# Optimization experiments

Measured on AMD Instinct MI355X. Metric: run time of the kernel, lower is better.

The kernel has to match this reference:

```python
import jax, jax.numpy as jnp
import numpy as np

E, K = 8, 2            # num_experts, top_k
D, H = 1024, 4096      # d_model, expert_hidden_dim
B, S = 4, 2048         # batch, seq
AUX_W = 0.01


def setup_inputs() -> dict:
    key = jax.random.key(0)
    k0, k1, k2, k3 = jax.random.split(key, 4)
    return {
        "x": jax.random.normal(k0, (B, S, D), jnp.float32),
        "router_w": jax.random.normal(k1, (D, E), jnp.float32) * 0.02,  # normal(0.02) init per MoERouter
        "router_b": jnp.zeros((E,), jnp.float32),
        "w_up": jax.random.normal(k2, (E, D, H), jnp.float32) * (1.0 / np.sqrt(D)),
        "b_up": jnp.zeros((E, H), jnp.float32),
        "w_down": jax.random.normal(k3, (E, H, D), jnp.float32) * (1.0 / np.sqrt(H)),
        "b_down": jnp.zeros((E, D), jnp.float32),
    }


def reference(x, router_w, router_b, w_up, b_up, w_down, b_down):
    # Router
    logits = x @ router_w + router_b                       # (B,S,E)
    router_probs = jax.nn.softmax(logits, axis=-1)         # (B,S,E)
    topk_logits, topk_idx = jax.lax.top_k(logits, K)       # (B,S,K)
    topk_p = jax.nn.softmax(topk_logits, axis=-1)          # (B,S,K)

    # Dense all-expert MLP (matches original: every expert computed on every token)
    h = jax.nn.gelu(jnp.einsum('bsd,edh->bseh', x, w_up) + b_up)   # (B,S,E,H)
    all_out = jnp.einsum('bseh,ehd->bsed', h, w_down) + b_down     # (B,S,E,D)

    # Top-k gather + weighted combine
    sel = jnp.take_along_axis(all_out, topk_idx[..., None], axis=2)  # (B,S,K,D)
    output = jnp.sum(topk_p[..., None] * sel, axis=2)                # (B,S,D)

    # Load-balancing aux loss (Switch/Mixtral formulation)
    counts = jnp.zeros((E,), jnp.float32).at[topk_idx.reshape(-1)].add(1.0)
    fraction = counts / (B * S * K)
    prob_mean = router_probs.mean(axis=(0, 1))
    aux_loss = E * jnp.sum(fraction * prob_mean) * AUX_W
    return output, aux_loss, router_probs
```

## Files before the change

### kernel.cpp

```cpp
#include <hip/hip_runtime.h>
#include <hip/hip_bf16.h>
#include <stdint.h>

constexpr int NT = 8192;
constexpr int NE = 8;
constexpr int ND = 1024;
constexpr int NH = 4096;

typedef __attribute__((ext_vector_type(8))) short short8;
typedef __attribute__((ext_vector_type(4))) float f32x4;

constexpr size_t O_XBF  = 0;
constexpr size_t O_WUPT = O_XBF  + (size_t)NT * ND * 2;
constexpr size_t O_WDNT = O_WUPT + (size_t)NE * NH * ND * 2;
constexpr size_t O_HBUF = O_WDNT + (size_t)NE * ND * NH * 2;
constexpr size_t O_STOK = O_HBUF + (size_t)NT * 2 * NH * 2;
constexpr size_t O_SP   = O_STOK + (size_t)NT * 2 * 4;
constexpr size_t O_TKE  = O_SP   + (size_t)NT * 2 * 4;
constexpr size_t O_TKP  = O_TKE  + (size_t)NT * 2 * 4;
constexpr size_t O_CTRL = O_TKP  + (size_t)NT * 2 * 4;
constexpr size_t O_TLUP = O_CTRL + 272;
constexpr size_t O_TLDN = O_TLUP + 144 * 4;

__device__ __forceinline__ void gl_lds16(const void* g, void* l) {
  using GP = char __attribute__((address_space(1))) *;
  using LP = char __attribute__((address_space(3))) *;
  __builtin_amdgcn_global_load_lds((GP)(uintptr_t)g, (LP)(uint32_t)(uintptr_t)l, 16, 0, 0);
}

__device__ __forceinline__ float fast_gelu(float x) {
  float u  = 0.7978845608028654f * (x + 0.044715f * x * x * x);
  float ex = __expf(2.0f * u);
  float th = 1.0f - 2.0f / (ex + 1.0f);
  return 0.5f * x * (1.0f + th);
}

__global__ __launch_bounds__(256) void moe_router(
    const float* __restrict__ x, const float* __restrict__ rw, const float* __restrict__ rb,
    __hip_bfloat16* __restrict__ xbf,
    float* __restrict__ probs_out, int* __restrict__ topk_e, float* __restrict__ topk_p,
    int* __restrict__ cnt_ek, float* __restrict__ probsum)
{
  __shared__ float ps[NE];
  __shared__ int cs[16];
  const int tid = threadIdx.x;
  if (tid < NE) ps[tid] = 0.f;
  if (tid < 16) cs[tid] = 0;
  __syncthreads();
  const int lane = tid & 63, wv = tid >> 6;
  for (int it = 0; it < 8; ++it) {
    const int t = blockIdx.x * 4 + wv + it * 1024;
    const float* xr = x + (size_t)t * ND;
    float acc[NE] = {};
#pragma unroll 4
    for (int j = 0; j < 16; ++j) {
      const int d = j * 64 + lane;
      const float xv = xr[d];
      xbf[(size_t)t * ND + d] = __float2bfloat16(xv);
      const float* w = rw + (size_t)d * NE;
#pragma unroll
      for (int ee = 0; ee < NE; ++ee) acc[ee] += xv * w[ee];
    }
#pragma unroll
    for (int ee = 0; ee < NE; ++ee)
#pragma unroll
      for (int off = 32; off >= 1; off >>= 1)
        acc[ee] += __shfl_down(acc[ee], off, 64);
    if (lane == 0) {
      float lg[NE];
#pragma unroll
      for (int ee = 0; ee < NE; ++ee) lg[ee] = acc[ee] + rb[ee];
      float mx = lg[0];
#pragma unroll
      for (int ee = 1; ee < NE; ++ee) mx = fmaxf(mx, lg[ee]);
      float s = 0.f, pe[NE];
#pragma unroll
      for (int ee = 0; ee < NE; ++ee) { pe[ee] = __expf(lg[ee] - mx); s += pe[ee]; }
      const float inv = 1.f / s;
#pragma unroll
      for (int ee = 0; ee < NE; ++ee) {
        const float pr = pe[ee] * inv;
        probs_out[(size_t)t * NE + ee] = pr;
        atomicAdd(&ps[ee], pr);
      }
      int i1 = 0; float l1 = lg[0];
#pragma unroll
      for (int ee = 1; ee < NE; ++ee) if (lg[ee] > l1) { l1 = lg[ee]; i1 = ee; }
      int i2 = 0; float l2 = -3.0e38f;
#pragma unroll
      for (int ee = 0; ee < NE; ++ee) if (ee != i1 && lg[ee] > l2) { l2 = lg[ee]; i2 = ee; }
      const float e2 = __expf(l2 - l1);
      const float dn = 1.f + e2;
      topk_e[t * 2]     = i1;  topk_e[t * 2 + 1] = i2;
      topk_p[t * 2]     = 1.f / dn;
      topk_p[t * 2 + 1] = e2 / dn;
      atomicAdd(&cs[i1 * 2], 1);
      atomicAdd(&cs[i2 * 2 + 1], 1);
    }
  }
  __syncthreads();
  if (tid < NE) atomicAdd(&probsum[tid], ps[tid]);
  if (tid < 16) atomicAdd(&cnt_ek[tid], cs[tid]);
}

__global__ void moe_finalize(const int* __restrict__ cnt_ek, int* __restrict__ off_ek,
                             const float* __restrict__ probsum, float* __restrict__ aux_out,
                             int* __restrict__ ntiles, int* __restrict__ tl_up,
                             int* __restrict__ tl_dn)
{
  if (threadIdx.x == 0 && blockIdx.x == 0) {
    int run = 0;
    for (int i = 0; i < 16; ++i) { off_ek[i] = run; run += cnt_ek[i]; }
    float aux = 0.f;
    for (int ee = 0; ee < NE; ++ee) {
      float frac = (float)(cnt_ek[2 * ee] + cnt_ek[2 * ee + 1]) / (float)(NT * 2);
      aux += frac * (probsum[ee] / (float)NT);
    }
    aux_out[0] = (float)NE * aux * 0.01f;
    int ntu = 0;
    for (int e = 0; e < NE; ++e) {
      const int c = cnt_ek[2 * e] + cnt_ek[2 * e + 1];
      for (int mb = 0; mb < (c + 127) / 128; ++mb) tl_up[ntu++] = (e << 16) | mb;
    }
    ntiles[0] = ntu;
    for (int kp = 0; kp < 2; ++kp) {
      int nt = 0;
      for (int e = 0; e < NE; ++e) {
        const int c = cnt_ek[2 * e + kp];
        for (int mb = 0; mb < (c + 127) / 128; ++mb) tl_dn[kp * 80 + nt++] = (e << 16) | mb;
      }
      ntiles[1 + kp] = nt;
    }
  }
}

__global__ __launch_bounds__(256) void moe_scatter(
    const int* __restrict__ topk_e, const float* __restrict__ topk_p,
    const int* __restrict__ off_ek, int* __restrict__ fill_ek,
    int* __restrict__ slot_token, float* __restrict__ slot_p)
{
  const int t = blockIdx.x * 256 + threadIdx.x;
  if (t >= NT) return;
#pragma unroll
  for (int k = 0; k < 2; ++k) {
    const int ee = topk_e[t * 2 + k];
    const int id = ee * 2 + k;
    const int r = atomicAdd(&fill_ek[id], 1);
    const int slot = off_ek[id] + r;
    slot_token[slot] = t;
    slot_p[slot] = topk_p[t * 2 + k];
  }
}

__global__ __launch_bounds__(256) void moe_transpose_cast(
    const float* __restrict__ in, __hip_bfloat16* __restrict__ outp, int Adim, int Bdim)
{
  __shared__ unsigned short tile[64 * 66];
  const int e = blockIdx.z;
  const int b0 = blockIdx.x * 64, a0 = blockIdx.y * 64;
  const float* ip = in + (size_t)e * Adim * Bdim + (size_t)a0 * Bdim + b0;
  const int c4 = (threadIdx.x & 15) * 4;
  const int r0 = threadIdx.x >> 4;
#pragma unroll
  for (int i = 0; i < 4; ++i) {
    const int r = r0 + i * 16;
    const float4 v = *(const float4*)(ip + (size_t)r * Bdim + c4);
    ushort4 u;
    u.x = __hip_bfloat16_raw(__float2bfloat16(v.x)).x;
    u.y = __hip_bfloat16_raw(__float2bfloat16(v.y)).x;
    u.z = __hip_bfloat16_raw(__float2bfloat16(v.z)).x;
    u.w = __hip_bfloat16_raw(__float2bfloat16(v.w)).x;
    *(ushort4*)&tile[r * 66 + c4] = u;
  }
  __syncthreads();
  unsigned short* op = (unsigned short*)outp + (size_t)e * Bdim * Adim + (size_t)b0 * Adim + a0;
  const int cc  = threadIdx.x >> 2;
  const int rr0 = (threadIdx.x & 3) * 16;
  unsigned short u[16];
#pragma unroll
  for (int i = 0; i < 16; ++i) u[i] = tile[(rr0 + i) * 66 + cc];
  *(short8*)(op + (size_t)cc * Adim + rr0)     = *(short8*)&u[0];
  *(short8*)(op + (size_t)cc * Adim + rr0 + 8) = *(short8*)&u[8];
}

__global__ __launch_bounds__(512, 5) void moe_gemm_up(
    const __hip_bfloat16* __restrict__ xbf,
    const __hip_bfloat16* __restrict__ wupT,
    const float* __restrict__ b_up,
    const int* __restrict__ slot_token,
    const int* __restrict__ cnt_ek, const int* __restrict__ off_ek,
    const int* __restrict__ ntiles, const int* __restrict__ tl_up,
    __hip_bfloat16* __restrict__ hbuf)
{
  if ((int)blockIdx.y >= ntiles[0]) return;
  const int tl = tl_up[blockIdx.y];
  const int e = tl >> 16, mb = tl & 0xffff;
  const int cnt = cnt_ek[2 * e] + cnt_ek[2 * e + 1];
  const int base = off_ek[2 * e];
  const int m0 = mb * 128;
  const int n0 = blockIdx.x * 128;
  const int valid = (cnt - m0 < 128) ? (cnt - m0) : 128;

  __shared__ __align__(16) __hip_bfloat16 As[128 * 32];
  __shared__ __align__(16) __hip_bfloat16 Bs[128 * 32];

  const int tid = threadIdx.x;
  const int lane = tid & 63, wv = tid >> 6;

  const int ra = tid >> 2;
  const int kc = ((tid & 3) ^ ((ra >> 1) & 3)) * 8;
  const int sa = base + ((m0 + ra < cnt) ? (m0 + ra) : (cnt - 1));
  const __hip_bfloat16* ga = xbf + (size_t)slot_token[sa] * ND + kc;
  const __hip_bfloat16* gb = wupT + ((size_t)e * NH + n0 + ra) * ND + kc;
  char* lA = (char*)As + tid * 16;
  char* lB = (char*)Bs + tid * 16;

  const int wm = (wv >> 2) * 64, wn = (wv & 3) * 32;
  const int l15 = lane & 15, q = lane >> 4;
  const int ssw = (q ^ ((l15 >> 1) & 3)) * 16;
  const char* rA = (const char*)As + (wm + l15) * 64 + ssw;
  const char* rB = (const char*)Bs + (wn + l15) * 64 + ssw;

  f32x4 acc[4][2] = {};

  for (int kk = 0; kk < ND; kk += 32) {
    __syncthreads();
    gl_lds16(ga + kk, lA);
    gl_lds16(gb + kk, lB);
    __syncthreads();
    short8 af[4], bfr[2];
#pragma unroll
    for (int i = 0; i < 4; ++i) af[i]  = *(const short8*)(rA + i * 1024);
#pragma unroll
    for (int i = 0; i < 2; ++i) bfr[i] = *(const short8*)(rB + i * 1024);
#pragma unroll
    for (int mt = 0; mt < 4; ++mt)
#pragma unroll
      for (int nt = 0; nt < 2; ++nt)
        acc[mt][nt] = __builtin_amdgcn_mfma_f32_16x16x32_bf16(af[mt], bfr[nt], acc[mt][nt], 0, 0, 0);
  }

#pragma unroll
  for (int mt = 0; mt < 4; ++mt) {
#pragma unroll
    for (int rr = 0; rr < 4; ++rr) {
      const int row = wm + mt * 16 + q * 4 + rr;
      if (row < valid) {
        const size_t rbase = (size_t)(base + m0 + row) * NH;
#pragma unroll
        for (int nt = 0; nt < 2; ++nt) {
          const int col = n0 + wn + nt * 16 + l15;
          const float v = acc[mt][nt][rr] + b_up[e * NH + col];
          hbuf[rbase + col] = __float2bfloat16(fast_gelu(v));
        }
      }
    }
  }
}

__global__ __launch_bounds__(512, 5) void moe_gemm_down(
    const __hip_bfloat16* __restrict__ hbuf,
    const __hip_bfloat16* __restrict__ wdnT,
    const float* __restrict__ b_down,
    const int* __restrict__ slot_token, const float* __restrict__ slot_p,
    const int* __restrict__ cnt_ek, const int* __restrict__ off_ek,
    const int* __restrict__ ntiles, const int* __restrict__ tl_dn,
    float* __restrict__ out, int kpos)
{
  if ((int)blockIdx.y >= ntiles[1 + kpos]) return;
  const int tl = tl_dn[kpos * 80 + blockIdx.y];
  const int e = tl >> 16, mb = tl & 0xffff;
  const int id = 2 * e + kpos;
  const int cnt = cnt_ek[id];
  const int base = off_ek[id];
  const int m0 = mb * 128;
  const int n0 = blockIdx.x * 128;
  const int valid = (cnt - m0 < 128) ? (cnt - m0) : 128;

  __shared__ __align__(16) __hip_bfloat16 As[128 * 32];
  __shared__ __align__(16) __hip_bfloat16 Bs[128 * 32];

  const int tid = threadIdx.x;
  const int lane = tid & 63, wv = tid >> 6;

  const int ra = tid >> 2;
  const int kc = ((tid & 3) ^ ((ra >> 1) & 3)) * 8;
  const int sa = base + ((m0 + ra < cnt) ? (m0 + ra) : (cnt - 1));
  const __hip_bfloat16* ga = hbuf + (size_t)sa * NH + kc;
  const __hip_bfloat16* gb = wdnT + ((size_t)e * ND + n0 + ra) * NH + kc;
  char* lA = (char*)As + tid * 16;
  char* lB = (char*)Bs + tid * 16;

  const int wm = (wv >> 2) * 64, wn = (wv & 3) * 32;
  const int l15 = lane & 15, q = lane >> 4;
  const int ssw = (q ^ ((l15 >> 1) & 3)) * 16;
  const char* rA = (const char*)As + (wm + l15) * 64 + ssw;
  const char* rB = (const char*)Bs + (wn + l15) * 64 + ssw;

  f32x4 acc[4][2] = {};

  for (int kk = 0; kk < NH; kk += 32) {
    __syncthreads();
    gl_lds16(ga + kk, lA);
    gl_lds16(gb + kk, lB);
    __syncthreads();
    short8 af[4], bfr[2];
#pragma unroll
    for (int i = 0; i < 4; ++i) af[i]  = *(const short8*)(rA + i * 1024);
#pragma unroll
    for (int i = 0; i < 2; ++i) bfr[i] = *(const short8*)(rB + i * 1024);
#pragma unroll
    for (int mt = 0; mt < 4; ++mt)
#pragma unroll
      for (int nt = 0; nt < 2; ++nt)
        acc[mt][nt] = __builtin_amdgcn_mfma_f32_16x16x32_bf16(af[mt], bfr[nt], acc[mt][nt], 0, 0, 0);
  }

#pragma unroll
  for (int mt = 0; mt < 4; ++mt) {
#pragma unroll
    for (int rr = 0; rr < 4; ++rr) {
      const int row = wm + mt * 16 + q * 4 + rr;
      if (row < valid) {
        const int slot = base + m0 + row;
        const int tok = slot_token[slot];
        const float p = slot_p[slot];
        const size_t obase = (size_t)tok * ND;
#pragma unroll
        for (int nt = 0; nt < 2; ++nt) {
          const int col = n0 + wn + nt * 16 + l15;
          const float v = (acc[mt][nt][rr] + b_down[e * ND + col]) * p;
          if (kpos == 0) out[obase + col] = v;
          else           out[obase + col] += v;
        }
      }
    }
  }
}

extern "C" void kernel_launch(void* const* d_in, const int* in_sizes, int n_in,
                              void* d_out, int out_size, void* d_ws, size_t ws_size,
                              hipStream_t stream) {
  (void)in_sizes; (void)n_in; (void)out_size; (void)ws_size;
  const float* x   = (const float*)d_in[0];
  const float* rw  = (const float*)d_in[1];
  const float* rb  = (const float*)d_in[2];
  const float* wup = (const float*)d_in[3];
  const float* bup = (const float*)d_in[4];
  const float* wdn = (const float*)d_in[5];
  const float* bdn = (const float*)d_in[6];
  float* out = (float*)d_out;

  char* ws = (char*)d_ws;
  __hip_bfloat16* xbf  = (__hip_bfloat16*)(ws + O_XBF);
  __hip_bfloat16* wupT = (__hip_bfloat16*)(ws + O_WUPT);
  __hip_bfloat16* wdnT = (__hip_bfloat16*)(ws + O_WDNT);
  __hip_bfloat16* hbuf = (__hip_bfloat16*)(ws + O_HBUF);
  int*   slot_token = (int*)(ws + O_STOK);
  float* slot_p     = (float*)(ws + O_SP);
  int*   topk_e     = (int*)(ws + O_TKE);
  float* topk_p     = (float*)(ws + O_TKP);
  int*   cnt_ek  = (int*)(ws + O_CTRL);
  int*   fill_ek = (int*)(ws + O_CTRL + 64);
  float* probsum = (float*)(ws + O_CTRL + 128);
  int*   off_ek  = (int*)(ws + O_CTRL + 192);
  int*   ntiles  = (int*)(ws + O_CTRL + 256);
  int*   tl_up   = (int*)(ws + O_TLUP);
  int*   tl_dn   = (int*)(ws + O_TLDN);

  hipMemsetAsync(ws + O_CTRL, 0, 272, stream);

  moe_transpose_cast<<<dim3(NH / 64, ND / 64, NE), 256, 0, stream>>>(wup, wupT, ND, NH);
  moe_transpose_cast<<<dim3(ND / 64, NH / 64, NE), 256, 0, stream>>>(wdn, wdnT, NH, ND);

  moe_router<<<256, 256, 0, stream>>>(x, rw, rb, xbf, out + (size_t)NT * ND + 1,
                                      topk_e, topk_p, cnt_ek, probsum);
  moe_finalize<<<1, 64, 0, stream>>>(cnt_ek, off_ek, probsum, out + (size_t)NT * ND,
                                     ntiles, tl_up, tl_dn);
  moe_scatter<<<NT / 256, 256, 0, stream>>>(topk_e, topk_p, off_ek, fill_ek, slot_token, slot_p);

  moe_gemm_up<<<dim3(NH / 128, 144, 1), 512, 0, stream>>>(xbf, wupT, bup, slot_token,
                                                          cnt_ek, off_ek, ntiles, tl_up, hbuf);
  moe_gemm_down<<<dim3(ND / 128, 80, 1), 512, 0, stream>>>(hbuf, wdnT, bdn, slot_token, slot_p,
                                                           cnt_ek, off_ek, ntiles, tl_dn, out, 0);
  moe_gemm_down<<<dim3(ND / 128, 80, 1), 512, 0, stream>>>(hbuf, wdnT, bdn, slot_token, slot_p,
                                                           cnt_ek, off_ek, ntiles, tl_dn, out, 1);
}
```

Before: 933.2 us.

## Use 192x192x64 tiles with 32x32 MFMA and merge down-proj launches via atomics

New measurement: 1.108 ms. 1.19x slower.

```diff
diff --git a/kernel.cpp b/kernel.cpp
--- a/kernel.cpp
+++ b/kernel.cpp
@@ -7,8 +7,13 @@
 constexpr int ND = 1024;
 constexpr int NH = 4096;
 
-typedef __attribute__((ext_vector_type(8))) short short8;
-typedef __attribute__((ext_vector_type(4))) float f32x4;
+constexpr int TM = 192;
+constexpr int TN = 192;
+constexpr int BK = 64;
+
+typedef __attribute__((ext_vector_type(8)))  short short8;
+typedef __attribute__((ext_vector_type(16))) float f32x16;
+typedef __attribute__((ext_vector_type(4)))  float f32x4;
 
 constexpr size_t O_XBF  = 0;
 constexpr size_t O_WUPT = O_XBF  + (size_t)NT * ND * 2;
@@ -20,7 +25,7 @@
 constexpr size_t O_TKP  = O_TKE  + (size_t)NT * 2 * 4;
 constexpr size_t O_CTRL = O_TKP  + (size_t)NT * 2 * 4;
 constexpr size_t O_TLUP = O_CTRL + 272;
-constexpr size_t O_TLDN = O_TLUP + 144 * 4;
+constexpr size_t O_TLDN = O_TLUP + 96 * 4;
 
 __device__ __forceinline__ void gl_lds16(const void* g, void* l) {
   using GP = char __attribute__((address_space(1))) *;
@@ -120,17 +125,16 @@
     int ntu = 0;
     for (int e = 0; e < NE; ++e) {
       const int c = cnt_ek[2 * e] + cnt_ek[2 * e + 1];
-      for (int mb = 0; mb < (c + 127) / 128; ++mb) tl_up[ntu++] = (e << 16) | mb;
+      for (int mb = 0; mb < (c + TM - 1) / TM; ++mb) tl_up[ntu++] = (e << 20) | mb;
     }
     ntiles[0] = ntu;
-    for (int kp = 0; kp < 2; ++kp) {
-      int nt = 0;
+    int nt = 0;
+    for (int kp = 0; kp < 2; ++kp)
       for (int e = 0; e < NE; ++e) {
         const int c = cnt_ek[2 * e + kp];
-        for (int mb = 0; mb < (c + 127) / 128; ++mb) tl_dn[kp * 80 + nt++] = (e << 16) | mb;
+        for (int mb = 0; mb < (c + TM - 1) / TM; ++mb) tl_dn[nt++] = (e << 20) | (kp << 16) | mb;
       }
-      ntiles[1 + kp] = nt;
-    }
+    ntiles[1] = nt;
   }
 }
 
@@ -183,7 +187,7 @@
   *(short8*)(op + (size_t)cc * Adim + rr0 + 8) = *(short8*)&u[8];
 }
 
-__global__ __launch_bounds__(512, 5) void moe_gemm_up(
+__global__ __launch_bounds__(256, 2) void moe_gemm_up(
     const __hip_bfloat16* __restrict__ xbf,
     const __hip_bfloat16* __restrict__ wupT,
     const float* __restrict__ b_up,
@@ -194,144 +198,181 @@
 {
   if ((int)blockIdx.y >= ntiles[0]) return;
   const int tl = tl_up[blockIdx.y];
-  const int e = tl >> 16, mb = tl & 0xffff;
+  const int e = tl >> 20, mb = tl & 0xffff;
   const int cnt = cnt_ek[2 * e] + cnt_ek[2 * e + 1];
   const int base = off_ek[2 * e];
-  const int m0 = mb * 128;
-  const int n0 = blockIdx.x * 128;
-  const int valid = (cnt - m0 < 128) ? (cnt - m0) : 128;
-
-  __shared__ __align__(16) __hip_bfloat16 As[128 * 32];
-  __shared__ __align__(16) __hip_bfloat16 Bs[128 * 32];
+  const int m0 = mb * TM;
+  const int n0 = blockIdx.x * TN;
+  const int valid = (cnt - m0 < TM) ? (cnt - m0) : TM;
+
+  __shared__ __align__(16) __hip_bfloat16 As[TM * BK];
+  __shared__ __align__(16) __hip_bfloat16 Bs[TN * BK];
 
   const int tid = threadIdx.x;
   const int lane = tid & 63, wv = tid >> 6;
 
-  const int ra = tid >> 2;
-  const int kc = ((tid & 3) ^ ((ra >> 1) & 3)) * 8;
-  const int sa = base + ((m0 + ra < cnt) ? (m0 + ra) : (cnt - 1));
-  const __hip_bfloat16* ga = xbf + (size_t)slot_token[sa] * ND + kc;
-  const __hip_bfloat16* gb = wupT + ((size_t)e * NH + n0 + ra) * ND + kc;
+  const __hip_bfloat16* aptr[6];
+  const __hip_bfloat16* bptr[6];
+#pragma unroll
+  for (int j = 0; j < 6; ++j) {
+    const int ci = tid + 256 * j;
+    const int row = ci >> 3;
+    const int kc = (((ci & 7) ^ (row & 7))) * 8;
+    int sr = m0 + row; if (sr >= cnt) sr = cnt - 1;
+    aptr[j] = xbf + (size_t)slot_token[base + sr] * ND + kc;
+    int br = n0 + row; if (br >= NH) br = NH - 1;
+    bptr[j] = wupT + ((size_t)e * NH + br) * ND + kc;
+  }
   char* lA = (char*)As + tid * 16;
   char* lB = (char*)Bs + tid * 16;
 
-  const int wm = (wv >> 2) * 64, wn = (wv & 3) * 32;
-  const int l15 = lane & 15, q = lane >> 4;
-  const int ssw = (q ^ ((l15 >> 1) & 3)) * 16;
-  const char* rA = (const char*)As + (wm + l15) * 64 + ssw;
-  const char* rB = (const char*)Bs + (wn + l15) * 64 + ssw;
-
-  f32x4 acc[4][2] = {};
-
-  for (int kk = 0; kk < ND; kk += 32) {
+  const int wm = (wv >> 1) * 96, wn = (wv & 1) * 96;
+  const int l31 = lane & 31, h = lane >> 5, swz = l31 & 7;
+  const int arb = (wm + l31) * (BK * 2);
+  const int brb = (wn + l31) * (BK * 2);
+
+  f32x16 acc[3][3] = {};
+
+  for (int kk = 0; kk < ND; kk += BK) {
     __syncthreads();
-    gl_lds16(ga + kk, lA);
-    gl_lds16(gb + kk, lB);
+#pragma unroll
+    for (int j = 0; j < 6; ++j) { gl_lds16(aptr[j], lA + j * 4096); aptr[j] += BK; }
+#pragma unroll
+    for (int j = 0; j < 6; ++j) { gl_lds16(bptr[j], lB + j * 4096); bptr[j] += BK; }
     __syncthreads();
-    short8 af[4], bfr[2];
-#pragma unroll
-    for (int i = 0; i < 4; ++i) af[i]  = *(const short8*)(rA + i * 1024);
-#pragma unroll
-    for (int i = 0; i < 2; ++i) bfr[i] = *(const short8*)(rB + i * 1024);
-#pragma unroll
-    for (int mt = 0; mt < 4; ++mt)
-#pragma unroll
-      for (int nt = 0; nt < 2; ++nt)
-        acc[mt][nt] = __builtin_amdgcn_mfma_f32_16x16x32_bf16(af[mt], bfr[nt], acc[mt][nt], 0, 0, 0);
-  }
-
-#pragma unroll
-  for (int mt = 0; mt < 4; ++mt) {
-#pragma unroll
-    for (int rr = 0; rr < 4; ++rr) {
-      const int row = wm + mt * 16 + q * 4 + rr;
+#pragma unroll
+    for (int s = 0; s < 4; ++s) {
+      const int sl = ((((s << 1) | h) ^ swz) << 4);
+      short8 af[3], bfr[3];
+#pragma unroll
+      for (int i = 0; i < 3; ++i) af[i]  = *(const short8*)((const char*)As + arb + i * 4096 + sl);
+#pragma unroll
+      for (int i = 0; i < 3; ++i) bfr[i] = *(const short8*)((const char*)Bs + brb + i * 4096 + sl);
+#pragma unroll
+      for (int mt = 0; mt < 3; ++mt)
+#pragma unroll
+        for (int nt = 0; nt < 3; ++nt)
+          acc[mt][nt] = __builtin_amdgcn_mfma_f32_32x32x16_bf16(af[mt], bfr[nt], acc[mt][nt], 0, 0, 0);
+    }
+  }
+
+  float bias[3];
+#pragma unroll
+  for (int nt = 0; nt < 3; ++nt) {
+    const int col = n0 + wn + nt * 32 + l31;
+    bias[nt] = (col < NH) ? b_up[e * NH + col] : 0.f;
+  }
+#pragma unroll
+  for (int mt = 0; mt < 3; ++mt) {
+#pragma unroll
+    for (int r = 0; r < 16; ++r) {
+      const int rowl = (r & 3) + ((r >> 2) << 3) + (h << 2);
+      const int row = wm + mt * 32 + rowl;
       if (row < valid) {
         const size_t rbase = (size_t)(base + m0 + row) * NH;
 #pragma unroll
-        for (int nt = 0; nt < 2; ++nt) {
-          const int col = n0 + wn + nt * 16 + l15;
-          const float v = acc[mt][nt][rr] + b_up[e * NH + col];
-          hbuf[rbase + col] = __float2bfloat16(fast_gelu(v));
+        for (int nt = 0; nt < 3; ++nt) {
+          const int col = n0 + wn + nt * 32 + l31;
+          if (col < NH)
+            hbuf[rbase + col] = __float2bfloat16(fast_gelu(acc[mt][nt][r] + bias[nt]));
         }
       }
     }
   }
 }
 
-__global__ __launch_bounds__(512, 5) void moe_gemm_down(
+__global__ __launch_bounds__(256, 2) void moe_gemm_down(
     const __hip_bfloat16* __restrict__ hbuf,
     const __hip_bfloat16* __restrict__ wdnT,
     const float* __restrict__ b_down,
     const int* __restrict__ slot_token, const float* __restrict__ slot_p,
     const int* __restrict__ cnt_ek, const int* __restrict__ off_ek,
     const int* __restrict__ ntiles, const int* __restrict__ tl_dn,
-    float* __restrict__ out, int kpos)
-{
-  if ((int)blockIdx.y >= ntiles[1 + kpos]) return;
-  const int tl = tl_dn[kpos * 80 + blockIdx.y];
-  const int e = tl >> 16, mb = tl & 0xffff;
-  const int id = 2 * e + kpos;
+    float* __restrict__ out)
+{
+  if ((int)blockIdx.y >= ntiles[1]) return;
+  const int tl = tl_dn[blockIdx.y];
+  const int e = tl >> 20, kp = (tl >> 16) & 0xF, mb = tl & 0xffff;
+  const int id = 2 * e + kp;
   const int cnt = cnt_ek[id];
   const int base = off_ek[id];
-  const int m0 = mb * 128;
-  const int n0 = blockIdx.x * 128;
-  const int valid = (cnt - m0 < 128) ? (cnt - m0) : 128;
-
-  __shared__ __align__(16) __hip_bfloat16 As[128 * 32];
-  __shared__ __align__(16) __hip_bfloat16 Bs[128 * 32];
+  const int m0 = mb * TM;
+  const int n0 = blockIdx.x * TN;
+  const int valid = (cnt - m0 < TM) ? (cnt - m0) : TM;
+
+  __shared__ __align__(16) __hip_bfloat16 As[TM * BK];
+  __shared__ __align__(16) __hip_bfloat16 Bs[TN * BK];
 
   const int tid = threadIdx.x;
   const int lane = tid & 63, wv = tid >> 6;
 
-  const int ra = tid >> 2;
-  const int kc = ((tid & 3) ^ ((ra >> 1) & 3)) * 8;
-  const int sa = base + ((m0 + ra < cnt) ? (m0 + ra) : (cnt - 1));
-  const __hip_bfloat16* ga = hbuf + (size_t)sa * NH + kc;
-  const __hip_bfloat16* gb = wdnT + ((size_t)e * ND + n0 + ra) * NH + kc;
+  const __hip_bfloat16* aptr[6];
+  const __hip_bfloat16* bptr[6];
+#pragma unroll
+  for (int j = 0; j < 6; ++j) {
+    const int ci = tid + 256 * j;
+    const int row = ci >> 3;
+    const int kc = (((ci & 7) ^ (row & 7))) * 8;
+    int sr = m0 + row; if (sr >= cnt) sr = cnt - 1;
+    aptr[j] = hbuf + (size_t)(base + sr) * NH + kc;
+    int br = n0 + row; if (br >= ND) br = ND - 1;
+    bptr[j] = wdnT + ((size_t)e * ND + br) * NH + kc;
+  }
   char* lA = (char*)As + tid * 16;
   char* lB = (char*)Bs + tid * 16;
 
-  const int wm = (wv >> 2) * 64, wn = (wv & 3) * 32;
-  const int l15 = lane & 15, q = lane >> 4;
-  const int ssw = (q ^ ((l15 >> 1) & 3)) * 16;
-  const char* rA = (const char*)As + (wm + l15) * 64 + ssw;
-  const char* rB = (const char*)Bs + (wn + l15) * 64 + ssw;
-
-  f32x4 acc[4][2] = {};
-
-  for (int kk = 0; kk < NH; kk += 32) {
+  const int wm = (wv >> 1) * 96, wn = (wv & 1) * 96;
+  const int l31 = lane & 31, h = lane >> 5, swz = l31 & 7;
+  const int arb = (wm + l31) * (BK * 2);
+  const int brb = (wn + l31) * (BK * 2);
+
+  f32x16 acc[3][3] = {};
+
+  for (int kk = 0; kk < NH; kk += BK) {
     __syncthreads();
-    gl_lds16(ga + kk, lA);
-    gl_lds16(gb + kk, lB);
+#pragma unroll
+    for (int j = 0; j < 6; ++j) { gl_lds16(aptr[j], lA + j * 4096); aptr[j] += BK; }
+#pragma unroll
+    for (int j = 0; j < 6; ++j) { gl_lds16(bptr[j], lB + j * 4096); bptr[j] += BK; }
     __syncthreads();
-    short8 af[4], bfr[2];
-#pragma unroll
-    for (int i = 0; i < 4; ++i) af[i]  = *(const short8*)(rA + i * 1024);
-#pragma unroll
-    for (int i = 0; i < 2; ++i) bfr[i] = *(const short8*)(rB + i * 1024);
-#pragma unroll
-    for (int mt = 0; mt < 4; ++mt)
-#pragma unroll
-      for (int nt = 0; nt < 2; ++nt)
-        acc[mt][nt] = __builtin_amdgcn_mfma_f32_16x16x32_bf16(af[mt], bfr[nt], acc[mt][nt], 0, 0, 0);
-  }
-
-#pragma unroll
-  for (int mt = 0; mt < 4; ++mt) {
-#pragma unroll
-    for (int rr = 0; rr < 4; ++rr) {
-      const int row = wm + mt * 16 + q * 4 + rr;
+#pragma unroll
+    for (int s = 0; s < 4; ++s) {
+      const int sl = ((((s << 1) | h) ^ swz) << 4);
+      short8 af[3], bfr[3];
+#pragma unroll
+      for (int i = 0; i < 3; ++i) af[i]  = *(const short8*)((const char*)As + arb + i * 4096 + sl);
+#pragma unroll
+      for (int i = 0; i < 3; ++i) bfr[i] = *(const short8*)((const char*)Bs + brb + i * 4096 + sl);
+#pragma unroll
+      for (int mt = 0; mt < 3; ++mt)
+#pragma unroll
+        for (int nt = 0; nt < 3; ++nt)
+          acc[mt][nt] = __builtin_amdgcn_mfma_f32_32x32x16_bf16(af[mt], bfr[nt], acc[mt][nt], 0, 0, 0);
+    }
+  }
+
+  float bias[3];
+#pragma unroll
+  for (int nt = 0; nt < 3; ++nt) {
+    const int col = n0 + wn + nt * 32 + l31;
+    bias[nt] = (col < ND) ? b_down[e * ND + col] : 0.f;
+  }
+#pragma unroll
+  for (int mt = 0; mt < 3; ++mt) {
+#pragma unroll
+    for (int r = 0; r < 16; ++r) {
+      const int rowl = (r & 3) + ((r >> 2) << 3) + (h << 2);
+      const int row = wm + mt * 32 + rowl;
       if (row < valid) {
         const int slot = base + m0 + row;
         const int tok = slot_token[slot];
         const float p = slot_p[slot];
         const size_t obase = (size_t)tok * ND;
 #pragma unroll
-        for (int nt = 0; nt < 2; ++nt) {
-          const int col = n0 + wn + nt * 16 + l15;
-          const float v = (acc[mt][nt][rr] + b_down[e * ND + col]) * p;
-          if (kpos == 0) out[obase + col] = v;
-          else           out[obase + col] += v;
+        for (int nt = 0; nt < 3; ++nt) {
+          const int col = n0 + wn + nt * 32 + l31;
+          if (col < ND)
+            atomicAdd(&out[obase + col], (acc[mt][nt][r] + bias[nt]) * p);
         }
       }
     }
@@ -369,6 +410,7 @@
   int*   tl_dn   = (int*)(ws + O_TLDN);
 
   hipMemsetAsync(ws + O_CTRL, 0, 272, stream);
+  hipMemsetAsync(out, 0, (size_t)NT * ND * sizeof(float), stream);
 
   moe_transpose_cast<<<dim3(NH / 64, ND / 64, NE), 256, 0, stream>>>(wup, wupT, ND, NH);
   moe_transpose_cast<<<dim3(ND / 64, NH / 64, NE), 256, 0, stream>>>(wdn, wdnT, NH, ND);
@@ -379,10 +421,8 @@
                                      ntiles, tl_up, tl_dn);
   moe_scatter<<<NT / 256, 256, 0, stream>>>(topk_e, topk_p, off_ek, fill_ek, slot_token, slot_p);
 
-  moe_gemm_up<<<dim3(NH / 128, 144, 1), 512, 0, stream>>>(xbf, wupT, bup, slot_token,
-                                                          cnt_ek, off_ek, ntiles, tl_up, hbuf);
-  moe_gemm_down<<<dim3(ND / 128, 80, 1), 512, 0, stream>>>(hbuf, wdnT, bdn, slot_token, slot_p,
-                                                           cnt_ek, off_ek, ntiles, tl_dn, out, 0);
-  moe_gemm_down<<<dim3(ND / 128, 80, 1), 512, 0, stream>>>(hbuf, wdnT, bdn, slot_token, slot_p,
-                                                           cnt_ek, off_ek, ntiles, tl_dn, out, 1);
-}
+  moe_gemm_up<<<dim3((NH + TN - 1) / TN, 96, 1), 256, 0, stream>>>(
+      xbf, wupT, bup, slot_token, cnt_ek, off_ek, ntiles, tl_up, hbuf);
+  moe_gemm_down<<<dim3((ND + TN - 1) / TN, 112, 1), 256, 0, stream>>>(
+      hbuf, wdnT, bdn, slot_token, slot_p, cnt_ek, off_ek, ntiles, tl_dn, out);
+}
```
